# Kernel optimization log

Measured on AMD Instinct MI355X. Metric: run time of the kernel, lower is better.

Reference implementation:

```python
import jax, jax.numpy as jnp
import numpy as np

G, N_PER_G, S, DEG, EMB, LAYERS = 64, 64, 8, 4, 128, 5


def _build_structure():
    """Ring graphs (degree DEG) with per-root windows of S nodes.
    Returns all integer index arrays for the tuple-sparse conv."""
    N = G * N_PER_G
    P = N * S          # (i, j) pairs
    T = P * S          # (i, j, k) tuples, k fastest
    deltas = np.array([1, 2, -1, -2])
    roots = np.arange(N)
    gbase = (roots // N_PER_G) * N_PER_G
    # window(i): S consecutive nodes in the same graph
    win = ((roots % N_PER_G)[:, None] + np.arange(S)) % N_PER_G + gbase[:, None]  # [N,S]
    tupleid0 = np.repeat(roots, S * S)
    tupleid1 = np.repeat(win.ravel(), S)
    # valid (k-offset, delta) combos so that l = k + delta stays inside window
    ok_g, di_g = np.meshgrid(np.arange(S), np.arange(DEG), indexing='ij')
    ol = ok_g + deltas[di_g]
    m = (ol >= 0) & (ol < S)
    ok_v, di_v, ol_v = ok_g[m], di_g[m], ol[m]        # [26]
    pairs = np.arange(P)
    msg_dst = (pairs[:, None] * S + ok_v[None, :]).ravel()
    msg_src = (pairs[:, None] * S + ol_v[None, :]).ravel()
    i_of_pair = pairs // S
    k_glob = ((i_of_pair % N_PER_G)[:, None] + ok_v[None, :]) % N_PER_G \
             + ((i_of_pair // N_PER_G) * N_PER_G)[:, None]
    msg_edge = (k_glob * DEG + di_v[None, :]).ravel()  # edge id = u*DEG + delta_idx
    seg_pair = np.arange(T) // S   # tuple -> (i,j) pair
    seg_node = np.arange(P) // S   # pair  -> root node i
    batch = np.repeat(np.arange(G), N_PER_G)
    return N, P, T, tupleid0, tupleid1, msg_src, msg_dst, msg_edge, seg_pair, seg_node, batch


def setup_inputs() -> dict:
    rng = np.random.default_rng(0)
    N, P, T, t0, t1, ms, md, me, sp, sn, batch = _build_structure()
    E = N * DEG
    i32 = lambda a: jnp.asarray(a, jnp.int32)
    key = jax.random.key(0)
    ks = jax.random.split(key, 8)
    sc = 0.05
    inp = {
        'x': i32(rng.integers(0, 32, N)),
        'edge_attr': i32(rng.integers(0, 16, E)),
        'tuplefeat': i32(rng.integers(0, 16, (T, 2))),
        'batch': i32(batch),
        'tupleid0': i32(t0), 'tupleid1': i32(t1),
        'msg_src': i32(ms), 'msg_dst': i32(md), 'msg_edge': i32(me),
        'seg_pair': i32(sp), 'seg_node': i32(sn),
        'num_graphs': G,
        'emb_x': jax.random.normal(ks[0], (32, EMB), jnp.float32) * sc,
        'emb_ea': jax.random.normal(ks[1], (16, EMB), jnp.float32) * sc,
        'emb_tf': jax.random.normal(ks[2], (16, EMB // 2), jnp.float32) * sc,
        'w_ti': jax.random.normal(ks[3], (EMB, EMB), jnp.float32) * sc,
        'b_ti': jnp.zeros((EMB,), jnp.float32),
        'w_conv': jax.random.normal(ks[4], (LAYERS, EMB, EMB), jnp.float32) * sc,
        'b_conv': jnp.zeros((LAYERS, EMB), jnp.float32),
        'w_pred': jax.random.normal(ks[5], (EMB, 1), jnp.float32) * sc,
        'b_pred': jnp.zeros((1,), jnp.float32),
    }
    return inp


def reference(x, edge_attr, tuplefeat, batch, tupleid0, tupleid1,
              msg_src, msg_dst, msg_edge, seg_pair, seg_node, num_graphs,
              emb_x, emb_ea, emb_tf, w_ti, b_ti, w_conv, b_conv, w_pred, b_pred):
    T = tuplefeat.shape[0]
    N = x.shape[0]
    P = seg_node.shape[0]
    # InputEncoder
    xe = emb_x[x]                                   # [N, E]
    ea = emb_ea[edge_attr]                          # [E_edges, E]
    tf = emb_tf[tuplefeat].reshape(T, -1)           # [T, 2, E/2] -> [T, E]
    # tupleinit: x[t0] * lin(x)[t1] * tuplefeat
    Xv = xe[tupleid0] * (xe @ w_ti + b_ti)[tupleid1] * tf   # [T, E]

    def layer(carry, wb):
        w, b = wb
        msgs = carry[msg_src] * ea[msg_edge]                         # [M, E]
        agg = jax.ops.segment_sum(msgs, msg_dst, num_segments=T)      # [T, E]
        return carry + jax.nn.relu(agg @ w + b), None                 # residual

    Xv, _ = jax.lax.scan(layer, Xv, (w_conv, b_conv))
    # pooling2tuple (max over k), pooling2nodes (sum over j), npool (sum over batch)
    pair = jax.ops.segment_max(Xv, seg_pair, num_segments=P)          # [P, E]
    node = jax.ops.segment_sum(pair, seg_node, num_segments=N)        # [N, E]
    graph = jax.ops.segment_sum(node, batch, num_segments=num_graphs) # [G, E]
    return graph @ w_pred + b_pred                                    # [G, 1]
```

## Files before the change

### kernel.cpp

```cpp
#include <hip/hip_runtime.h>
#include <hip/hip_bf16.h>

#define EMB 128

typedef __attribute__((ext_vector_type(8))) short short8;
typedef __attribute__((ext_vector_type(4))) float floatx4;
typedef __attribute__((ext_vector_type(2))) float v2f;

static constexpr int OKv[26] = {0,0,1,1,1,2,2,2,2,3,3,3,3,4,4,4,4,5,5,5,5,6,6,6,7,7};
static constexpr int DIv[26] = {0,1,0,1,2,0,1,2,3,0,1,2,3,0,1,2,3,0,1,2,3,0,2,3,2,3};
static constexpr int OLv[26] = {1,2,2,3,0,3,4,1,0,4,5,2,1,5,6,3,2,6,7,4,3,7,5,4,6,5};

__device__ __forceinline__ v2f ldv2(const float* p) { return *(const v2f*)p; }

__device__ __forceinline__ unsigned bf16_rne_hi(float x) {
  unsigned u = __float_as_uint(x);
  return (u + 0x7FFFu + ((u >> 16) & 1u)) & 0xFFFF0000u;
}
__device__ __forceinline__ unsigned cvt_pk_bf16(float a, float b) {
  __hip_bfloat162 h = __float22bfloat162_rn(make_float2(a, b));
  unsigned r; __builtin_memcpy(&r, &h, 4); return r;
}

union FragU { unsigned u[4]; uint4 q; short8 v; };


__global__ __launch_bounds__(512) void prep_kernel(
    const float* __restrict__ emb_x,
    const float* __restrict__ w_ti,
    const float* __restrict__ b_ti,
    const float* __restrict__ w_conv,
    const float* __restrict__ b_pred,
    float* __restrict__ lin32,
    uint4* __restrict__ wfrag,
    float* __restrict__ out) {
  const int b = blockIdx.x, tid = threadIdx.x;
  if (b < 32) {
    __shared__ float red[4][EMB];
    const int e = tid & 127, fh = tid >> 7;
    const float* xr = emb_x + b * EMB;
    float s = 0.f;
    #pragma unroll 8
    for (int f = fh * 32; f < fh * 32 + 32; ++f)
      s = fmaf(xr[f], w_ti[f * EMB + e], s);
    red[fh][e] = s;
    __syncthreads();
    if (fh == 0)
      lin32[b * EMB + e] =
          b_ti[e] + ((red[0][e] + red[1][e]) + (red[2][e] + red[3][e]));
  } else if (b < 52) {
    const int id   = (b - 32) * 512 + tid;
    const int lane = id & 63;
    const int f    = id >> 6;
    const int u    = f & 7;
    const int t    = (f >> 3) & 3;
    const int l    = f >> 5;
    const int q    = lane >> 4, n = lane & 15;
    const int cN   = 2 * ((u >> 1) * 16 + n) + (u & 1);
    unsigned w[4] = {0u, 0u, 0u, 0u};
    #pragma unroll
    for (int j = 0; j < 8; ++j) {
      const int kk = t * 32 + q * 8 + j;
      const float val = w_conv[l * (EMB * EMB) + kk * EMB + cN];
      const unsigned bb = bf16_rne_hi(val);
      w[j >> 1] |= (j & 1) ? bb : (bb >> 16);
    }
    wfrag[id] = make_uint4(w[0], w[1], w[2], w[3]);
  } else {
    if (tid < 64) out[tid] = b_pred[0];
  }
}

__global__ __launch_bounds__(256, 2)
void i2gnn_mfma(
    const int* __restrict__ x,
    const int* __restrict__ edge_attr,
    const int* __restrict__ tuplefeat,
    const float* __restrict__ emb_x,
    const float* __restrict__ emb_tf,
    const float* __restrict__ emb_ea,
    const float* __restrict__ lin32,
    const float* __restrict__ b_conv,
    const float* __restrict__ w_pred,
    const uint4* __restrict__ wfrag,
    float* __restrict__ out)
{
  __shared__ __align__(16) unsigned fragA[2 * 64 * 68];
  __shared__ __align__(16) float eas[16 * EMB];

  const int tid = threadIdx.x;
  const int wv = tid >> 6, lane = tid & 63;
  const int m16 = lane & 15, q2 = lane >> 4;
  const int pc = wv * 16 + m16;
  const int c0 = pc * 2;

  const int i = blockIdx.x;
  const int ibase = i & ~63, io = i & 63;
  const int g = i >> 6;

  {
    const float4* src = (const float4*)emb_ea;
    float4* dst = (float4*)eas;
    dst[tid] = src[tid];
    dst[tid + 256] = src[tid + 256];
  }

  unsigned pk[4] = {0u, 0u, 0u, 0u};
  #pragma unroll
  for (int m = 0; m < 26; ++m) {
    const int kg = ibase + ((io + OKv[m]) & 63);
    const unsigned a = (unsigned)edge_attr[(kg << 2) + DIv[m]];
    pk[m >> 3] |= a << ((m & 7) * 4);
  }

  const int xi = x[i];
  const v2f xe = ldv2(emb_x + xi * EMB + c0);
  v2f lj[2];
  #pragma unroll
  for (int ps = 0; ps < 2; ++ps) {
    const int jn = ibase + ((io + 2 * q2 + ps) & 63);
    lj[ps] = ldv2(lin32 + x[jn] * EMB + c0);
  }
  v2f X2[4][4];
  #pragma unroll
  for (int mt = 0; mt < 4; ++mt) {
    const int ps = mt & 1, kb = (mt >> 1) * 4;
    const int t0 = (i * 8 + 2 * q2 + ps) << 3;
    const v2f xl = xe * lj[ps];
    #pragma unroll
    for (int r = 0; r < 4; ++r) {
      const int2 tf2 = *(const int2*)(tuplefeat + 2 * (t0 + kb + r));
      const int row = (c0 < 64) ? tf2.x : tf2.y;
      const v2f tf = ldv2(emb_tf + row * 64 + (c0 & 63));
      X2[mt][r] = xl * tf;
    }
  }

  __syncthreads();

  const float* eabase = eas + c0;

  for (int l = 0; l < 5; ++l) {
    unsigned* fbuf = fragA + (l & 1) * 4352;

    v2f acc[2][8];
    #pragma unroll
    for (int ps = 0; ps < 2; ++ps)
      #pragma unroll
      for (int k = 0; k < 8; ++k) acc[ps][k] = (v2f){0.f, 0.f};
    #pragma unroll
    for (int m = 0; m < 26; ++m) {
      const unsigned attr = (pk[m >> 3] >> ((m & 7) * 4)) & 15u;
      const v2f e = ldv2(eabase + attr * EMB);
      const int ok = OKv[m], ol = OLv[m];
      const int mtb = 2 * (ol >> 2), rl = ol & 3;
      acc[0][ok] += X2[mtb + 0][rl] * e;
      acc[1][ok] += X2[mtb + 1][rl] * e;
    }
    #pragma unroll
    for (int ps = 0; ps < 2; ++ps)
      #pragma unroll
      for (int k = 0; k < 8; ++k) {
        const v2f a = acc[ps][k];
        const int row = (ps + 2 * (k >> 2)) * 16 + q2 * 4 + (k & 3);
        fbuf[row * 68 + pc] = cvt_pk_bf16(a.x, a.y);
      }

    FragU B0, B1;
    {
      const uint4* wp0 = wfrag + (((l * 4 + 0) * 8 + 2 * wv) << 6);
      B0.q = wp0[lane];  B1.q = wp0[64 + lane];
    }

    __syncthreads();

    floatx4 C[2][4];
    #pragma unroll
    for (int v = 0; v < 2; ++v)
      #pragma unroll
      for (int mt = 0; mt < 4; ++mt) C[v][mt] = (floatx4){0.f, 0.f, 0.f, 0.f};

    __builtin_amdgcn_s_setprio(1);
    #pragma unroll
    for (int kt = 0; kt < 4; ++kt) {
      FragU nB0, nB1;
      if (kt < 3) {
        const uint4* wpn = wfrag + (((l * 4 + kt + 1) * 8 + 2 * wv) << 6);
        nB0.q = wpn[lane];  nB1.q = wpn[64 + lane];
      }
      #pragma unroll
      for (int mt = 0; mt < 4; ++mt) {
        const unsigned* fa = fbuf + (mt * 16 + m16) * 68 + kt * 16 + q2 * 4;
        FragU Ah;
        Ah.q = *(const uint4*)fa;
        C[0][mt] = __builtin_amdgcn_mfma_f32_16x16x32_bf16(Ah.v, B0.v, C[0][mt], 0, 0, 0);
        C[1][mt] = __builtin_amdgcn_mfma_f32_16x16x32_bf16(Ah.v, B1.v, C[1][mt], 0, 0, 0);
      }
      if (kt < 3) { B0 = nB0; B1 = nB1; }
    }
    __builtin_amdgcn_s_setprio(0);

    const v2f bc = ldv2(b_conv + l * EMB + c0);
    #pragma unroll
    for (int mt = 0; mt < 4; ++mt)
      #pragma unroll
      for (int r = 0; r < 4; ++r) {
        v2f o; o.x = C[0][mt][r]; o.y = C[1][mt][r];
        o += bc;
        o.x = fmaxf(o.x, 0.f); o.y = fmaxf(o.y, 0.f);
        X2[mt][r] += o;
      }
  }

  const v2f wp = ldv2(w_pred + c0);
  v2f p0 = (v2f){-3.4e38f, -3.4e38f}, p1 = p0;
  #pragma unroll
  for (int r = 0; r < 4; ++r) {
    p0.x = fmaxf(p0.x, fmaxf(X2[0][r].x, X2[2][r].x));
    p0.y = fmaxf(p0.y, fmaxf(X2[0][r].y, X2[2][r].y));
    p1.x = fmaxf(p1.x, fmaxf(X2[1][r].x, X2[3][r].x));
    p1.y = fmaxf(p1.y, fmaxf(X2[1][r].y, X2[3][r].y));
  }
  const v2f ps = (p0 + p1) * wp;
  float s = ps.x + ps.y;
  #pragma unroll
  for (int off = 32; off; off >>= 1) s += __shfl_xor(s, off, 64);
  if (lane == 0) atomicAdd(out + g, s);
}

extern "C" void kernel_launch(void* const* d_in, const int* in_sizes, int n_in,
                              void* d_out, int out_size, void* d_ws, size_t ws_size,
                              hipStream_t stream) {
  const int*   x         = (const int*)d_in[0];
  const int*   edge_attr = (const int*)d_in[1];
  const int*   tuplefeat = (const int*)d_in[2];
  const float* emb_x     = (const float*)d_in[12];
  const float* emb_ea    = (const float*)d_in[13];
  const float* emb_tf    = (const float*)d_in[14];
  const float* w_ti      = (const float*)d_in[15];
  const float* b_ti      = (const float*)d_in[16];
  const float* w_conv    = (const float*)d_in[17];
  const float* b_conv    = (const float*)d_in[18];
  const float* w_pred    = (const float*)d_in[19];
  const float* b_pred    = (const float*)d_in[20];
  float* out = (float*)d_out;
  float* lin32 = (float*)d_ws;
  uint4* wfrag = (uint4*)((char*)d_ws + 32 * EMB * 4);

  hipLaunchKernelGGL(prep_kernel, dim3(53), dim3(512), 0, stream,
                     emb_x, w_ti, b_ti, w_conv, b_pred, lin32, wfrag, out);
  hipLaunchKernelGGL(i2gnn_mfma, dim3(4096), dim3(256), 0, stream,
                     x, edge_attr, tuplefeat, emb_x, emb_tf, emb_ea, lin32,
                     b_conv, w_pred, wfrag, out);
}
```

Before: 258.5 us.

## Process two root nodes per block and interleave their message and MFMA phases

```diff
diff --git a/kernel.cpp b/kernel.cpp
--- a/kernel.cpp
+++ b/kernel.cpp
@@ -71,6 +71,129 @@
   }
 }
 
+
+__device__ __forceinline__ void tuple_init(
+    int i, int ibase, int io,
+    const int* __restrict__ x, const int* __restrict__ edge_attr,
+    const int* __restrict__ tuplefeat,
+    const float* __restrict__ emb_x, const float* __restrict__ emb_tf,
+    const float* __restrict__ lin32,
+    int c0, int q2, v2f (&X2)[4][4], unsigned (&pk)[4])
+{
+  #pragma unroll
+  for (int m = 0; m < 26; ++m) {
+    const int kg = ibase + ((io + OKv[m]) & 63);
+    const unsigned a = (unsigned)edge_attr[(kg << 2) + DIv[m]];
+    pk[m >> 3] |= a << ((m & 7) * 4);
+  }
+  const int xi = x[i];
+  const v2f xe = ldv2(emb_x + xi * EMB + c0);
+  v2f lj[2];
+  #pragma unroll
+  for (int ps = 0; ps < 2; ++ps) {
+    const int jn = ibase + ((io + 2 * q2 + ps) & 63);
+    lj[ps] = ldv2(lin32 + x[jn] * EMB + c0);
+  }
+  #pragma unroll
+  for (int mt = 0; mt < 4; ++mt) {
+    const int ps = mt & 1, kb = (mt >> 1) * 4;
+    const int t0 = (i * 8 + 2 * q2 + ps) << 3;
+    const v2f xl = xe * lj[ps];
+    #pragma unroll
+    for (int r = 0; r < 4; ++r) {
+      const int2 tf2 = *(const int2*)(tuplefeat + 2 * (t0 + kb + r));
+      const int row = (c0 < 64) ? tf2.x : tf2.y;
+      const v2f tf = ldv2(emb_tf + row * 64 + (c0 & 63));
+      X2[mt][r] = xl * tf;
+    }
+  }
+}
+
+__device__ __forceinline__ void msg_pack(
+    const v2f (&X2)[4][4], const unsigned (&pk)[4],
+    const float* __restrict__ emb_ea,
+    int c0, int q2, int pc, unsigned* fbuf)
+{
+  v2f acc[2][8];
+  #pragma unroll
+  for (int ps = 0; ps < 2; ++ps)
+    #pragma unroll
+    for (int k = 0; k < 8; ++k) acc[ps][k] = (v2f){0.f, 0.f};
+  #pragma unroll
+  for (int m = 0; m < 26; ++m) {
+    const unsigned attr = (pk[m >> 3] >> ((m & 7) * 4)) & 15u;
+    const v2f e = ldv2(emb_ea + attr * EMB + c0);
+    const int ok = OKv[m], ol = OLv[m];
+    const int mtb = 2 * (ol >> 2), rl = ol & 3;
+    acc[0][ok] += X2[mtb + 0][rl] * e;
+    acc[1][ok] += X2[mtb + 1][rl] * e;
+  }
+  #pragma unroll
+  for (int ps = 0; ps < 2; ++ps)
+    #pragma unroll
+    for (int k = 0; k < 8; ++k) {
+      const v2f a = acc[ps][k];
+      const int row = (ps + 2 * (k >> 2)) * 16 + q2 * 4 + (k & 3);
+      fbuf[row * 68 + pc] = cvt_pk_bf16(a.x, a.y);
+    }
+}
+
+__device__ __forceinline__ void mfma_resid(
+    const unsigned* fbuf, const uint4* __restrict__ wfrag, int l,
+    int wv, int lane, int m16, int q2, v2f bc, v2f (&X2)[4][4])
+{
+  floatx4 C[2][4];
+  #pragma unroll
+  for (int v = 0; v < 2; ++v)
+    #pragma unroll
+    for (int mt = 0; mt < 4; ++mt) C[v][mt] = (floatx4){0.f, 0.f, 0.f, 0.f};
+  FragU B0, B1;
+  {
+    const uint4* wp0 = wfrag + (((l * 4 + 0) * 8 + 2 * wv) << 6);
+    B0.q = wp0[lane];  B1.q = wp0[64 + lane];
+  }
+  #pragma unroll
+  for (int kt = 0; kt < 4; ++kt) {
+    FragU nB0, nB1;
+    if (kt < 3) {
+      const uint4* wpn = wfrag + (((l * 4 + kt + 1) * 8 + 2 * wv) << 6);
+      nB0.q = wpn[lane];  nB1.q = wpn[64 + lane];
+    }
+    #pragma unroll
+    for (int mt = 0; mt < 4; ++mt) {
+      const unsigned* fa = fbuf + (mt * 16 + m16) * 68 + kt * 16 + q2 * 4;
+      FragU Ah;
+      Ah.q = *(const uint4*)fa;
+      C[0][mt] = __builtin_amdgcn_mfma_f32_16x16x32_bf16(Ah.v, B0.v, C[0][mt], 0, 0, 0);
+      C[1][mt] = __builtin_amdgcn_mfma_f32_16x16x32_bf16(Ah.v, B1.v, C[1][mt], 0, 0, 0);
+    }
+    if (kt < 3) { B0 = nB0; B1 = nB1; }
+  }
+  #pragma unroll
+  for (int mt = 0; mt < 4; ++mt)
+    #pragma unroll
+    for (int r = 0; r < 4; ++r) {
+      v2f o; o.x = C[0][mt][r]; o.y = C[1][mt][r];
+      o += bc;
+      o.x = fmaxf(o.x, 0.f); o.y = fmaxf(o.y, 0.f);
+      X2[mt][r] += o;
+    }
+}
+
+__device__ __forceinline__ float pool_dot(const v2f (&X2)[4][4], v2f wp)
+{
+  v2f p0 = (v2f){-3.4e38f, -3.4e38f}, p1 = p0;
+  #pragma unroll
+  for (int r = 0; r < 4; ++r) {
+    p0.x = fmaxf(p0.x, fmaxf(X2[0][r].x, X2[2][r].x));
+    p0.y = fmaxf(p0.y, fmaxf(X2[0][r].y, X2[2][r].y));
+    p1.x = fmaxf(p1.x, fmaxf(X2[1][r].x, X2[3][r].x));
+    p1.y = fmaxf(p1.y, fmaxf(X2[1][r].y, X2[3][r].y));
+  }
+  const v2f ps = (p0 + p1) * wp;
+  return ps.x + ps.y;
+}
+
 __global__ __launch_bounds__(256, 2)
 void i2gnn_mfma(
     const int* __restrict__ x,
@@ -85,8 +208,9 @@
     const uint4* __restrict__ wfrag,
     float* __restrict__ out)
 {
-  __shared__ __align__(16) unsigned fragA[2 * 64 * 68];
-  __shared__ __align__(16) float eas[16 * EMB];
+  __shared__ __align__(16) unsigned frag[2 * 64 * 68];
+  unsigned* bufA = frag;
+  unsigned* bufB = frag + 4352;
 
   const int tid = threadIdx.x;
   const int wv = tid >> 6, lane = tid & 63;
@@ -94,135 +218,38 @@
   const int pc = wv * 16 + m16;
   const int c0 = pc * 2;
 
-  const int i = blockIdx.x;
-  const int ibase = i & ~63, io = i & 63;
-  const int g = i >> 6;
-
-  {
-    const float4* src = (const float4*)emb_ea;
-    float4* dst = (float4*)eas;
-    dst[tid] = src[tid];
-    dst[tid + 256] = src[tid + 256];
-  }
-
-  unsigned pk[4] = {0u, 0u, 0u, 0u};
-  #pragma unroll
-  for (int m = 0; m < 26; ++m) {
-    const int kg = ibase + ((io + OKv[m]) & 63);
-    const unsigned a = (unsigned)edge_attr[(kg << 2) + DIv[m]];
-    pk[m >> 3] |= a << ((m & 7) * 4);
-  }
-
-  const int xi = x[i];
-  const v2f xe = ldv2(emb_x + xi * EMB + c0);
-  v2f lj[2];
-  #pragma unroll
-  for (int ps = 0; ps < 2; ++ps) {
-    const int jn = ibase + ((io + 2 * q2 + ps) & 63);
-    lj[ps] = ldv2(lin32 + x[jn] * EMB + c0);
-  }
-  v2f X2[4][4];
-  #pragma unroll
-  for (int mt = 0; mt < 4; ++mt) {
-    const int ps = mt & 1, kb = (mt >> 1) * 4;
-    const int t0 = (i * 8 + 2 * q2 + ps) << 3;
-    const v2f xl = xe * lj[ps];
-    #pragma unroll
-    for (int r = 0; r < 4; ++r) {
-      const int2 tf2 = *(const int2*)(tuplefeat + 2 * (t0 + kb + r));
-      const int row = (c0 < 64) ? tf2.x : tf2.y;
-      const v2f tf = ldv2(emb_tf + row * 64 + (c0 & 63));
-      X2[mt][r] = xl * tf;
-    }
-  }
-
+  const int iA = blockIdx.x * 2;
+  const int iB = iA + 1;
+  const int ibase = iA & ~63;
+  const int ioA = iA & 63, ioB = iB & 63;
+  const int g = iA >> 6;
+
+  v2f X2A[4][4], X2B[4][4];
+  unsigned pkA[4] = {0u,0u,0u,0u}, pkB[4] = {0u,0u,0u,0u};
+  tuple_init(iA, ibase, ioA, x, edge_attr, tuplefeat, emb_x, emb_tf, lin32,
+             c0, q2, X2A, pkA);
+  tuple_init(iB, ibase, ioB, x, edge_attr, tuplefeat, emb_x, emb_tf, lin32,
+             c0, q2, X2B, pkB);
+
+  msg_pack(X2A, pkA, emb_ea, c0, q2, pc, bufA);
   __syncthreads();
 
-  const float* eabase = eas + c0;
-
   for (int l = 0; l < 5; ++l) {
-    unsigned* fbuf = fragA + (l & 1) * 4352;
-
-    v2f acc[2][8];
-    #pragma unroll
-    for (int ps = 0; ps < 2; ++ps)
-      #pragma unroll
-      for (int k = 0; k < 8; ++k) acc[ps][k] = (v2f){0.f, 0.f};
-    #pragma unroll
-    for (int m = 0; m < 26; ++m) {
-      const unsigned attr = (pk[m >> 3] >> ((m & 7) * 4)) & 15u;
-      const v2f e = ldv2(eabase + attr * EMB);
-      const int ok = OKv[m], ol = OLv[m];
-      const int mtb = 2 * (ol >> 2), rl = ol & 3;
-      acc[0][ok] += X2[mtb + 0][rl] * e;
-      acc[1][ok] += X2[mtb + 1][rl] * e;
-    }
-    #pragma unroll
-    for (int ps = 0; ps < 2; ++ps)
-      #pragma unroll
-      for (int k = 0; k < 8; ++k) {
-        const v2f a = acc[ps][k];
-        const int row = (ps + 2 * (k >> 2)) * 16 + q2 * 4 + (k & 3);
-        fbuf[row * 68 + pc] = cvt_pk_bf16(a.x, a.y);
-      }
-
-    FragU B0, B1;
-    {
-      const uint4* wp0 = wfrag + (((l * 4 + 0) * 8 + 2 * wv) << 6);
-      B0.q = wp0[lane];  B1.q = wp0[64 + lane];
-    }
-
+    const v2f bc = ldv2(b_conv + l * EMB + c0);
+
+    mfma_resid(bufA, wfrag, l, wv, lane, m16, q2, bc, X2A);
+    msg_pack(X2B, pkB, emb_ea, c0, q2, pc, bufB);
     __syncthreads();
 
-    floatx4 C[2][4];
-    #pragma unroll
-    for (int v = 0; v < 2; ++v)
-      #pragma unroll
-      for (int mt = 0; mt < 4; ++mt) C[v][mt] = (floatx4){0.f, 0.f, 0.f, 0.f};
-
-    __builtin_amdgcn_s_setprio(1);
-    #pragma unroll
-    for (int kt = 0; kt < 4; ++kt) {
-      FragU nB0, nB1;
-      if (kt < 3) {
-        const uint4* wpn = wfrag + (((l * 4 + kt + 1) * 8 + 2 * wv) << 6);
-        nB0.q = wpn[lane];  nB1.q = wpn[64 + lane];
-      }
-      #pragma unroll
-      for (int mt = 0; mt < 4; ++mt) {
-        const unsigned* fa = fbuf + (mt * 16 + m16) * 68 + kt * 16 + q2 * 4;
-        FragU Ah;
-        Ah.q = *(const uint4*)fa;
-        C[0][mt] = __builtin_amdgcn_mfma_f32_16x16x32_bf16(Ah.v, B0.v, C[0][mt], 0, 0, 0);
-        C[1][mt] = __builtin_amdgcn_mfma_f32_16x16x32_bf16(Ah.v, B1.v, C[1][mt], 0, 0, 0);
-      }
-      if (kt < 3) { B0 = nB0; B1 = nB1; }
-    }
-    __builtin_amdgcn_s_setprio(0);
-
-    const v2f bc = ldv2(b_conv + l * EMB + c0);
-    #pragma unroll
-    for (int mt = 0; mt < 4; ++mt)
-      #pragma unroll
-      for (int r = 0; r < 4; ++r) {
-        v2f o; o.x = C[0][mt][r]; o.y = C[1][mt][r];
-        o += bc;
-        o.x = fmaxf(o.x, 0.f); o.y = fmaxf(o.y, 0.f);
-        X2[mt][r] += o;
-      }
+    mfma_resid(bufB, wfrag, l, wv, lane, m16, q2, bc, X2B);
+    if (l < 4) {
+      msg_pack(X2A, pkA, emb_ea, c0, q2, pc, bufA);
+      __syncthreads();
+    }
   }
 
   const v2f wp = ldv2(w_pred + c0);
-  v2f p0 = (v2f){-3.4e38f, -3.4e38f}, p1 = p0;
-  #pragma unroll
-  for (int r = 0; r < 4; ++r) {
-    p0.x = fmaxf(p0.x, fmaxf(X2[0][r].x, X2[2][r].x));
-    p0.y = fmaxf(p0.y, fmaxf(X2[0][r].y, X2[2][r].y));
-    p1.x = fmaxf(p1.x, fmaxf(X2[1][r].x, X2[3][r].x));
-    p1.y = fmaxf(p1.y, fmaxf(X2[1][r].y, X2[3][r].y));
-  }
-  const v2f ps = (p0 + p1) * wp;
-  float s = ps.x + ps.y;
+  float s = pool_dot(X2A, wp) + pool_dot(X2B, wp);
   #pragma unroll
   for (int off = 32; off; off >>= 1) s += __shfl_xor(s, off, 64);
   if (lane == 0) atomicAdd(out + g, s);
@@ -249,7 +276,7 @@
 
   hipLaunchKernelGGL(prep_kernel, dim3(53), dim3(512), 0, stream,
                      emb_x, w_ti, b_ti, w_conv, b_pred, lin32, wfrag, out);
-  hipLaunchKernelGGL(i2gnn_mfma, dim3(4096), dim3(256), 0, stream,
+  hipLaunchKernelGGL(i2gnn_mfma, dim3(2048), dim3(256), 0, stream,
                      x, edge_attr, tuplefeat, emb_x, emb_tf, emb_ea, lin32,
                      b_conv, w_pred, wfrag, out);
 }
```

Measured after the change: 242.1 us (median of 2 runs). 6.4% less time.
